# Kernel tuning notes

Hardware: AMD Instinct MI355X
Metric: run time of the kernel (lower is better)

Reference implementation:

```python
import jax, jax.numpy as jnp
import numpy as np

DIM = 768
N_HEADS = 12
HEAD_DIM = DIM // N_HEADS
HIDDEN = int(DIM * 4.0)
B, S = 4, 2048
EPS = 1e-6
SCALE = HEAD_DIM ** -0.5


def layer_norm(x, gamma, beta):
    mu = jnp.mean(x, axis=-1, keepdims=True)
    var = jnp.mean((x - mu) ** 2, axis=-1, keepdims=True)
    return (x - mu) * jax.lax.rsqrt(var + EPS) * gamma + beta


def setup_inputs() -> dict:
    key = jax.random.key(0)
    ks = jax.random.split(key, 8)
    x = jax.random.normal(ks[0], (B, S, DIM), dtype=jnp.float32)
    mask = jax.random.randint(ks[1], (B, 1, S, S), 0, 2, dtype=jnp.int32)
    sd = DIM ** -0.5
    return {
        "x": x,
        "mask": mask,
        "w_qkv": jax.random.normal(ks[2], (DIM, 3 * DIM), dtype=jnp.float32) * sd,
        "b_qkv": jnp.zeros((3 * DIM,), jnp.float32),
        "w_proj": jax.random.normal(ks[3], (DIM, DIM), dtype=jnp.float32) * sd,
        "b_proj": jnp.zeros((DIM,), jnp.float32),
        "g1": jnp.ones((DIM,), jnp.float32),
        "beta1": jnp.zeros((DIM,), jnp.float32),
        "g2": jnp.ones((DIM,), jnp.float32),
        "beta2": jnp.zeros((DIM,), jnp.float32),
        "w1": jax.random.normal(ks[4], (DIM, HIDDEN), dtype=jnp.float32) * sd,
        "b1": jnp.zeros((HIDDEN,), jnp.float32),
        "w2": jax.random.normal(ks[5], (HIDDEN, DIM), dtype=jnp.float32) * (HIDDEN ** -0.5),
        "b2": jnp.zeros((DIM,), jnp.float32),
    }


def reference(x, mask, w_qkv, b_qkv, w_proj, b_proj, g1, beta1, g2, beta2, w1, b1, w2, b2):
    # --- attention branch (pre-LN) ---
    h = layer_norm(x, g1, beta1)
    qkv = h @ w_qkv + b_qkv                              # (B,S,3*DIM)
    qkv = qkv.reshape(B, S, 3, N_HEADS, HEAD_DIM)
    q, k, v = (qkv[:, :, 0], qkv[:, :, 1], qkv[:, :, 2])  # (B,S,H,D)
    # scores: (B,H,S,S) -- materialized like the original
    dp = jnp.einsum("bqhd,bkhd->bhqk", q, k) * SCALE
    dp = jnp.where(mask == 0, jnp.float32(-10000.0), dp)
    attn = jax.nn.softmax(dp, axis=-1)
    wa = jnp.einsum("bhqk,bkhd->bqhd", attn, v).reshape(B, S, DIM)
    x = x + (wa @ w_proj + b_proj)
    # --- MLP branch (pre-LN) ---
    h = layer_norm(x, g2, beta2)
    h = jax.nn.gelu(h @ w1 + b1, approximate=False)
    x = x + (h @ w2 + b2)
    return x
```

## Files before the change

kernel.cpp:

```cpp
#include <hip/hip_runtime.h>
#include <math.h>

typedef __bf16 bf16;
typedef __bf16 bf16x8 __attribute__((ext_vector_type(8)));
typedef float f32x4 __attribute__((ext_vector_type(4)));

#define DIM 768
#define NH 12
#define HD 64
#define HID 3072
#define BB 4
#define SS 2048
#define SCALE_QK 0.125f
#define QPRESCALE 0.18033688011112042f

#define MFMA(a, b, c) __builtin_amdgcn_mfma_f32_16x16x32_bf16(a, b, c, 0, 0, 0)

__device__ __forceinline__ void gld16(const void* g, void* l) {
  __builtin_amdgcn_global_load_lds(
      (const __attribute__((address_space(1))) void*)g,
      (__attribute__((address_space(3))) void*)l, 16, 0, 0);
}

__global__ __launch_bounds__(256) void castT_kernel(
    const float* __restrict__ in, bf16* __restrict__ out, int R, int C) {
  __shared__ float tile[32][33];
  const int c0 = blockIdx.x * 32, r0 = blockIdx.y * 32;
  const int tx = threadIdx.x & 31, ty = threadIdx.x >> 5;
#pragma unroll
  for (int i = 0; i < 32; i += 8)
    tile[ty + i][tx] = in[(size_t)(r0 + ty + i) * C + c0 + tx];
  __syncthreads();
#pragma unroll
  for (int i = 0; i < 32; i += 8)
    out[(size_t)(c0 + ty + i) * R + r0 + tx] = (bf16)tile[tx][ty + i];
}

__global__ __launch_bounds__(256) void maskbits_kernel(
    const int* __restrict__ mask, unsigned* __restrict__ bits) {
  const int i = blockIdx.x * 256 + threadIdx.x;
  unsigned long long m = __ballot(mask[i] != 0);
  const int lane = threadIdx.x & 63;
  if (lane == 0) bits[i >> 5] = (unsigned)m;
  else if (lane == 32) bits[i >> 5] = (unsigned)(m >> 32);
}

__global__ __launch_bounds__(256) void ln_kernel(
    const float* __restrict__ x, const float* __restrict__ g,
    const float* __restrict__ beta, bf16* __restrict__ out) {
  const int row = blockIdx.x, t = threadIdx.x;
  const float* xr = x + (size_t)row * DIM;
  float v0 = xr[t], v1 = xr[t + 256], v2 = xr[t + 512];
  float s = v0 + v1 + v2;
  float s2 = v0 * v0 + v1 * v1 + v2 * v2;
#pragma unroll
  for (int d = 1; d < 64; d <<= 1) {
    s += __shfl_xor(s, d);
    s2 += __shfl_xor(s2, d);
  }
  __shared__ float red[8];
  const int wv = t >> 6, lane = t & 63;
  if (lane == 0) { red[wv] = s; red[wv + 4] = s2; }
  __syncthreads();
  s = red[0] + red[1] + red[2] + red[3];
  s2 = red[4] + red[5] + red[6] + red[7];
  const float mu = s * (1.0f / DIM);
  const float var = s2 * (1.0f / DIM) - mu * mu;
  const float r = rsqrtf(var + 1e-6f);
  bf16* o = out + (size_t)row * DIM;
  o[t] = (bf16)((v0 - mu) * r * g[t] + beta[t]);
  o[t + 256] = (bf16)((v1 - mu) * r * g[t + 256] + beta[t + 256]);
  o[t + 512] = (bf16)((v2 - mu) * r * g[t + 512] + beta[t + 512]);
}

enum { EPI_QKV = 0, EPI_PROJ = 1, EPI_FFN1 = 2, EPI_FFN2 = 3 };

template <int EPI, int K>
__global__ __launch_bounds__(256) void gemm_kernel(
    const bf16* __restrict__ A, const bf16* __restrict__ Bt,
    const float* __restrict__ bias, const float* __restrict__ res,
    void* __restrict__ o0, void* __restrict__ o1, void* __restrict__ o2) {
  __shared__ bf16 As[128 * 64];
  __shared__ bf16 Bs[128 * 64];
  const int tid = threadIdx.x;
  const int wv = tid >> 6, lane = tid & 63;
  const int quad = lane >> 4, l15 = lane & 15;
  const int lrow = lane >> 3, lcol = lane & 7;
  const int m0 = blockIdx.y * 128, n0 = blockIdx.x * 128;
  const int wm = (wv >> 1) * 64, wn = (wv & 1) * 64;

  f32x4 acc[4][4] = {};

  const int swz = (lcol ^ lrow) * 8;
  const bf16* Ag = A + (size_t)(m0 + wv * 32 + lrow) * K + swz;
  const bf16* Bg = Bt + (size_t)(n0 + wv * 32 + lrow) * K + swz;
  bf16* Al = As + (wv * 32) * 64;
  bf16* Bl = Bs + (wv * 32) * 64;

  for (int k0 = 0; k0 < K; k0 += 64) {
#pragma unroll
    for (int i = 0; i < 4; i++) {
      gld16(Ag + (size_t)(i * 8) * K + k0, Al + i * 8 * 64);
      gld16(Bg + (size_t)(i * 8) * K + k0, Bl + i * 8 * 64);
    }
    __syncthreads();
#pragma unroll
    for (int ks = 0; ks < 2; ks++) {
      bf16x8 af[4], bfr[4];
#pragma unroll
      for (int i = 0; i < 4; i++) {
        const int ra = wm + i * 16 + l15;
        af[i] = *(const bf16x8*)&As[ra * 64 + ((ks * 4 + quad) ^ (ra & 7)) * 8];
        const int rb = wn + i * 16 + l15;
        bfr[i] = *(const bf16x8*)&Bs[rb * 64 + ((ks * 4 + quad) ^ (rb & 7)) * 8];
      }
#pragma unroll
      for (int mi = 0; mi < 4; mi++)
#pragma unroll
        for (int ni = 0; ni < 4; ni++)
          acc[mi][ni] = MFMA(af[mi], bfr[ni], acc[mi][ni]);
    }
    __syncthreads();
  }

#pragma unroll
  for (int mi = 0; mi < 4; mi++) {
#pragma unroll
    for (int ni = 0; ni < 4; ni++) {
      const int n = n0 + wn + ni * 16 + l15;
      const float bv = bias[n];
      const int mb = m0 + wm + mi * 16 + quad * 4;
#pragma unroll
      for (int r = 0; r < 4; r++) {
        const int m = mb + r;
        const float val = acc[mi][ni][r] + bv;
        if (EPI == EPI_QKV) {
          const int which = n / 768;
          const int nn = n - which * 768;
          const int hh = nn >> 6, d = nn & 63;
          const int bb = m >> 11, s = m & 2047;
          if (which == 0) {
            ((bf16*)o0)[((size_t)(bb * NH + hh) * SS + s) * HD + d] =
                (bf16)(val * QPRESCALE);
          } else if (which == 1) {
            ((bf16*)o1)[((size_t)(bb * NH + hh) * SS + s) * HD + d] = (bf16)val;
          } else {
            ((bf16*)o2)[((size_t)(bb * NH + hh) * HD + d) * SS + s] = (bf16)val;
          }
        } else if (EPI == EPI_PROJ) {
          ((float*)o0)[(size_t)m * DIM + n] = res[(size_t)m * DIM + n] + val;
        } else if (EPI == EPI_FFN1) {
          const float ge = 0.5f * val * (1.0f + erff(val * 0.70710678118654752f));
          ((bf16*)o0)[(size_t)m * HID + n] = (bf16)ge;
        } else {
          ((float*)o0)[(size_t)m * DIM + n] = res[(size_t)m * DIM + n] + val;
        }
      }
    }
  }
}

__global__ __launch_bounds__(256) void attn_kernel(
    const bf16* __restrict__ q, const bf16* __restrict__ k,
    const bf16* __restrict__ vT, const unsigned* __restrict__ bits,
    bf16* __restrict__ wa) {
  const int b = blockIdx.z, h = blockIdx.y, q0 = blockIdx.x * 128;
  const int tid = threadIdx.x, wv = tid >> 6, lane = tid & 63;
  const int quad = lane >> 4, l15 = lane & 15;
  const int lrow = lane >> 3, lcol = lane & 7;

  __shared__ bf16 Ks[64 * 64];
  __shared__ bf16 Vs[64 * 64];
  __shared__ bf16 Ps[4][32 * 64];

  const bf16* qbh = q + (size_t)(b * NH + h) * SS * HD;
  const bf16* kbh = k + (size_t)(b * NH + h) * SS * HD;
  const bf16* vbh = vT + (size_t)(b * NH + h) * HD * SS;

  bf16x8 aq[2][2];
#pragma unroll
  for (int mi = 0; mi < 2; mi++)
#pragma unroll
    for (int ks = 0; ks < 2; ks++) {
      const int s = q0 + wv * 32 + mi * 16 + l15;
      aq[mi][ks] = *(const bf16x8*)&qbh[(size_t)s * HD + ks * 32 + quad * 8];
    }

  float lsum[2][4];
  f32x4 O[2][4] = {};
#pragma unroll
  for (int mi = 0; mi < 2; mi++)
#pragma unroll
    for (int r = 0; r < 4; r++) lsum[mi][r] = 0.0f;

  bf16* P = Ps[wv];
  const int swz = (lcol ^ lrow) * 8;
  const unsigned* bitrow =
      bits + (size_t)(b * SS + q0 + wv * 32 + quad * 4) * 64;

  for (int s0 = 0; s0 < SS; s0 += 64) {
#pragma unroll
    for (int i = 0; i < 2; i++) {
      const int r = wv * 16 + i * 8 + lrow;
      gld16(&kbh[(size_t)(s0 + r) * HD + swz], &Ks[(wv * 16 + i * 8) * 64]);
      gld16(&vbh[(size_t)r * SS + s0 + swz], &Vs[(wv * 16 + i * 8) * 64]);
    }

    unsigned long long ww[2][4];
#pragma unroll
    for (int mi = 0; mi < 2; mi++)
#pragma unroll
      for (int r = 0; r < 4; r++)
        ww[mi][r] = *(const unsigned long long*)&bitrow[(size_t)(mi * 16 + r) * 64 + (s0 >> 5)];

    __syncthreads();

    bf16x8 bk[4][2], bv[4][2];
#pragma unroll
    for (int ni = 0; ni < 4; ni++)
#pragma unroll
      for (int ks = 0; ks < 2; ks++) {
        const int rr = ni * 16 + l15;
        const int sl = ((ks * 4 + quad) ^ (rr & 7)) * 8;
        bk[ni][ks] = *(const bf16x8*)&Ks[rr * 64 + sl];
        bv[ni][ks] = *(const bf16x8*)&Vs[rr * 64 + sl];
      }

    f32x4 sc[2][4];
#pragma unroll
    for (int mi = 0; mi < 2; mi++)
#pragma unroll
      for (int ni = 0; ni < 4; ni++) {
        f32x4 a = {};
        a = MFMA(aq[mi][0], bk[ni][0], a);
        a = MFMA(aq[mi][1], bk[ni][1], a);
        sc[mi][ni] = a;
      }

#pragma unroll
    for (int mi = 0; mi < 2; mi++)
#pragma unroll
      for (int r = 0; r < 4; r++) {
        const unsigned long long sh = ww[mi][r] >> l15;
        const unsigned lo = (unsigned)sh, hi = (unsigned)(sh >> 32);
        float ls = lsum[mi][r];
#pragma unroll
        for (int ni = 0; ni < 4; ni++) {
          const unsigned bit =
              (ni == 0) ? (lo & 1u) : (ni == 1) ? ((lo >> 16) & 1u)
                        : (ni == 2) ? (hi & 1u) : ((hi >> 16) & 1u);
          float pv = __builtin_amdgcn_exp2f(sc[mi][ni][r]);
          pv = bit ? pv : 0.0f;
          sc[mi][ni][r] = pv;
          ls += pv;
        }
        lsum[mi][r] = ls;
      }

#pragma unroll
    for (int mi = 0; mi < 2; mi++)
#pragma unroll
      for (int ni = 0; ni < 4; ni++)
#pragma unroll
        for (int r = 0; r < 4; r++) {
          const int row = mi * 16 + quad * 4 + r;
          const int col = ni * 16 + l15;
          const int sl = (col >> 3) ^ (row & 7);
          P[row * 64 + sl * 8 + (col & 7)] = (bf16)sc[mi][ni][r];
        }

    bf16x8 ap[2][2];
#pragma unroll
    for (int mi = 0; mi < 2; mi++)
#pragma unroll
      for (int ks = 0; ks < 2; ks++) {
        const int rr = mi * 16 + l15;
        const int sl = ((ks * 4 + quad) ^ (rr & 7)) * 8;
        ap[mi][ks] = *(const bf16x8*)&P[rr * 64 + sl];
      }
#pragma unroll
    for (int mi = 0; mi < 2; mi++)
#pragma unroll
      for (int nd = 0; nd < 4; nd++) {
        O[mi][nd] = MFMA(ap[mi][0], bv[nd][0], O[mi][nd]);
        O[mi][nd] = MFMA(ap[mi][1], bv[nd][1], O[mi][nd]);
      }
    __syncthreads();
  }

  float rln[2][4];
#pragma unroll
  for (int mi = 0; mi < 2; mi++)
#pragma unroll
    for (int r = 0; r < 4; r++) {
      float ls = lsum[mi][r];
      ls += __shfl_xor(ls, 1);
      ls += __shfl_xor(ls, 2);
      ls += __shfl_xor(ls, 4);
      ls += __shfl_xor(ls, 8);
      rln[mi][r] = __builtin_amdgcn_rcpf(ls);
    }

#pragma unroll
  for (int mi = 0; mi < 2; mi++)
#pragma unroll
    for (int nd = 0; nd < 4; nd++)
#pragma unroll
      for (int r = 0; r < 4; r++) {
        const int s = q0 + wv * 32 + mi * 16 + quad * 4 + r;
        const int n = h * HD + nd * 16 + l15;
        wa[(size_t)(b * SS + s) * DIM + n] = (bf16)(O[mi][nd][r] * rln[mi][r]);
      }
}

extern "C" void kernel_launch(void* const* d_in, const int* in_sizes, int n_in,
                              void* d_out, int out_size, void* d_ws,
                              size_t ws_size, hipStream_t stream) {
  const float* x = (const float*)d_in[0];
  const int* mask = (const int*)d_in[1];
  const float* w_qkv = (const float*)d_in[2];
  const float* b_qkv = (const float*)d_in[3];
  const float* w_proj = (const float*)d_in[4];
  const float* b_proj = (const float*)d_in[5];
  const float* g1 = (const float*)d_in[6];
  const float* beta1 = (const float*)d_in[7];
  const float* g2 = (const float*)d_in[8];
  const float* beta2 = (const float*)d_in[9];
  const float* w1 = (const float*)d_in[10];
  const float* b1 = (const float*)d_in[11];
  const float* w2 = (const float*)d_in[12];
  const float* b2 = (const float*)d_in[13];
  float* out = (float*)d_out;

  char* p = (char*)d_ws;
  auto alloc = [&](size_t bytes) {
    char* r = p;
    p += (bytes + 1023) & ~(size_t)1023;
    return r;
  };
  bf16* wqkvT = (bf16*)alloc((size_t)2304 * 768 * 2);
  bf16* wprojT = (bf16*)alloc((size_t)768 * 768 * 2);
  bf16* w1T = (bf16*)alloc((size_t)3072 * 768 * 2);
  bf16* w2T = (bf16*)alloc((size_t)768 * 3072 * 2);
  unsigned* bits = (unsigned*)alloc((size_t)BB * SS * 64 * 4);
  bf16* h = (bf16*)alloc((size_t)8192 * 768 * 2);
  bf16* qb = (bf16*)alloc((size_t)8192 * 768 * 2);
  bf16* kb = (bf16*)alloc((size_t)8192 * 768 * 2);
  bf16* vtb = (bf16*)alloc((size_t)8192 * 768 * 2);
  bf16* wab = (bf16*)alloc((size_t)8192 * 768 * 2);
  float* x2 = (float*)alloc((size_t)8192 * 768 * 4);
  bf16* ffn1 = (bf16*)alloc((size_t)8192 * 3072 * 2);

  castT_kernel<<<dim3(2304 / 32, 768 / 32), 256, 0, stream>>>(w_qkv, wqkvT, 768, 2304);
  castT_kernel<<<dim3(768 / 32, 768 / 32), 256, 0, stream>>>(w_proj, wprojT, 768, 768);
  castT_kernel<<<dim3(3072 / 32, 768 / 32), 256, 0, stream>>>(w1, w1T, 768, 3072);
  castT_kernel<<<dim3(768 / 32, 3072 / 32), 256, 0, stream>>>(w2, w2T, 3072, 768);
  maskbits_kernel<<<(BB * SS * SS) / 256, 256, 0, stream>>>(mask, bits);
  ln_kernel<<<8192, 256, 0, stream>>>(x, g1, beta1, h);
  gemm_kernel<EPI_QKV, 768><<<dim3(2304 / 128, 8192 / 128), 256, 0, stream>>>(
      h, wqkvT, b_qkv, nullptr, qb, kb, vtb);
  attn_kernel<<<dim3(SS / 128, NH, BB), 256, 0, stream>>>(qb, kb, vtb, bits, wab);
  gemm_kernel<EPI_PROJ, 768><<<dim3(768 / 128, 8192 / 128), 256, 0, stream>>>(
      wab, wprojT, b_proj, x, x2, nullptr, nullptr);
  ln_kernel<<<8192, 256, 0, stream>>>(x2, g2, beta2, h);
  gemm_kernel<EPI_FFN1, 768><<<dim3(3072 / 128, 8192 / 128), 256, 0, stream>>>(
      h, w1T, b1, nullptr, ffn1, nullptr, nullptr);
  gemm_kernel<EPI_FFN2, 3072><<<dim3(768 / 128, 8192 / 128), 256, 0, stream>>>(
      ffn1, w2T, b2, x2, out, nullptr, nullptr);
}
```

Baseline: 541.9 us.

## Rewrite attention to keep P in registers via transposed MFMA, merge weight casts

The attention kernel now computes S^T by swapping the MFMA operands, so each lane holds one query row's probabilities. It feeds them straight into 16x16x16 MFMAs against V, which drops the LDS staging of K, V and P and removes both block barriers. K and V fragments are loaded directly from global memory per wave rather than shared through LDS, which raises global/L2 traffic per block. The four weight cast-transpose launches are merged into one kernel, and the V^T store in the QKV epilogue is packed into 8-byte writes.

Result: slower. 671.8 us (+24.0%).

```diff
diff --git a/kernel.cpp b/kernel.cpp
--- a/kernel.cpp
+++ b/kernel.cpp
@@ -1,8 +1,10 @@
 #include <hip/hip_runtime.h>
+#include <hip/hip_bf16.h>
 #include <math.h>
 
 typedef __bf16 bf16;
 typedef __bf16 bf16x8 __attribute__((ext_vector_type(8)));
+typedef short bf16x4s __attribute__((ext_vector_type(4)));
 typedef float f32x4 __attribute__((ext_vector_type(4)));
 
 #define DIM 768
@@ -15,6 +17,8 @@
 #define QPRESCALE 0.18033688011112042f
 
 #define MFMA(a, b, c) __builtin_amdgcn_mfma_f32_16x16x32_bf16(a, b, c, 0, 0, 0)
+#define MFMA16(a, b, c) \
+  __builtin_amdgcn_mfma_f32_16x16x16bf16_1k(a, b, c, 0, 0, 0)
 
 __device__ __forceinline__ void gld16(const void* g, void* l) {
   __builtin_amdgcn_global_load_lds(
@@ -22,10 +26,32 @@
       (__attribute__((address_space(3))) void*)l, 16, 0, 0);
 }
 
-__global__ __launch_bounds__(256) void castT_kernel(
-    const float* __restrict__ in, bf16* __restrict__ out, int R, int C) {
+__device__ __forceinline__ unsigned pk2(float a, float b) {
+  union {
+    bf16 h[2];
+    unsigned u;
+  } t;
+  t.h[0] = (bf16)a;
+  t.h[1] = (bf16)b;
+  return t.u;
+}
+
+__global__ __launch_bounds__(256) void castT_all_kernel(
+    const float* __restrict__ s0, bf16* __restrict__ d0,
+    const float* __restrict__ s1, bf16* __restrict__ d1,
+    const float* __restrict__ s2, bf16* __restrict__ d2,
+    const float* __restrict__ s3, bf16* __restrict__ d3) {
   __shared__ float tile[32][33];
-  const int c0 = blockIdx.x * 32, r0 = blockIdx.y * 32;
+  int id = blockIdx.x;
+  const float* in;
+  bf16* out;
+  int R, C, loc;
+  if (id < 1728) { in = s0; out = d0; R = 768; C = 2304; loc = id; }
+  else if (id < 2304) { in = s1; out = d1; R = 768; C = 768; loc = id - 1728; }
+  else if (id < 4608) { in = s2; out = d2; R = 768; C = 3072; loc = id - 2304; }
+  else { in = s3; out = d3; R = 3072; C = 768; loc = id - 4608; }
+  const int cb = C >> 5;
+  const int c0 = (loc % cb) * 32, r0 = (loc / cb) * 32;
   const int tx = threadIdx.x & 31, ty = threadIdx.x >> 5;
 #pragma unroll
   for (int i = 0; i < 32; i += 8)
@@ -130,31 +156,47 @@
       const int n = n0 + wn + ni * 16 + l15;
       const float bv = bias[n];
       const int mb = m0 + wm + mi * 16 + quad * 4;
-#pragma unroll
-      for (int r = 0; r < 4; r++) {
-        const int m = mb + r;
-        const float val = acc[mi][ni][r] + bv;
-        if (EPI == EPI_QKV) {
-          const int which = n / 768;
-          const int nn = n - which * 768;
-          const int hh = nn >> 6, d = nn & 63;
-          const int bb = m >> 11, s = m & 2047;
-          if (which == 0) {
-            ((bf16*)o0)[((size_t)(bb * NH + hh) * SS + s) * HD + d] =
-                (bf16)(val * QPRESCALE);
-          } else if (which == 1) {
-            ((bf16*)o1)[((size_t)(bb * NH + hh) * SS + s) * HD + d] = (bf16)val;
-          } else {
-            ((bf16*)o2)[((size_t)(bb * NH + hh) * HD + d) * SS + s] = (bf16)val;
-          }
-        } else if (EPI == EPI_PROJ) {
-          ((float*)o0)[(size_t)m * DIM + n] = res[(size_t)m * DIM + n] + val;
-        } else if (EPI == EPI_FFN1) {
-          const float ge = 0.5f * val * (1.0f + erff(val * 0.70710678118654752f));
-          ((bf16*)o0)[(size_t)m * HID + n] = (bf16)ge;
+      float val[4];
+#pragma unroll
+      for (int r = 0; r < 4; r++) val[r] = acc[mi][ni][r] + bv;
+      if (EPI == EPI_QKV) {
+        const int which = n / 768;
+        const int nn = n - which * 768;
+        const int hh = nn >> 6, d = nn & 63;
+        const int bb = mb >> 11, s = mb & 2047;
+        if (which == 0) {
+#pragma unroll
+          for (int r = 0; r < 4; r++)
+            ((bf16*)o0)[((size_t)(bb * NH + hh) * SS + s + r) * HD + d] =
+                (bf16)(val[r] * QPRESCALE);
+        } else if (which == 1) {
+#pragma unroll
+          for (int r = 0; r < 4; r++)
+            ((bf16*)o1)[((size_t)(bb * NH + hh) * SS + s + r) * HD + d] =
+                (bf16)val[r];
         } else {
-          ((float*)o0)[(size_t)m * DIM + n] = res[(size_t)m * DIM + n] + val;
+          uint2 pv;
+          pv.x = pk2(val[0], val[1]);
+          pv.y = pk2(val[2], val[3]);
+          *(uint2*)&((bf16*)o2)[((size_t)(bb * NH + hh) * HD + d) * SS + s] = pv;
         }
+      } else if (EPI == EPI_PROJ) {
+#pragma unroll
+        for (int r = 0; r < 4; r++)
+          ((float*)o0)[(size_t)(mb + r) * DIM + n] =
+              res[(size_t)(mb + r) * DIM + n] + val[r];
+      } else if (EPI == EPI_FFN1) {
+#pragma unroll
+        for (int r = 0; r < 4; r++) {
+          const float ge =
+              0.5f * val[r] * (1.0f + erff(val[r] * 0.70710678118654752f));
+          ((bf16*)o0)[(size_t)(mb + r) * HID + n] = (bf16)ge;
+        }
+      } else {
+#pragma unroll
+        for (int r = 0; r < 4; r++)
+          ((float*)o0)[(size_t)(mb + r) * DIM + n] =
+              res[(size_t)(mb + r) * DIM + n] + val[r];
       }
     }
   }
@@ -167,11 +209,6 @@
   const int b = blockIdx.z, h = blockIdx.y, q0 = blockIdx.x * 128;
   const int tid = threadIdx.x, wv = tid >> 6, lane = tid & 63;
   const int quad = lane >> 4, l15 = lane & 15;
-  const int lrow = lane >> 3, lcol = lane & 7;
-
-  __shared__ bf16 Ks[64 * 64];
-  __shared__ bf16 Vs[64 * 64];
-  __shared__ bf16 Ps[4][32 * 64];
 
   const bf16* qbh = q + (size_t)(b * NH + h) * SS * HD;
   const bf16* kbh = k + (size_t)(b * NH + h) * SS * HD;
@@ -186,131 +223,89 @@
       aq[mi][ks] = *(const bf16x8*)&qbh[(size_t)s * HD + ks * 32 + quad * 8];
     }
 
-  float lsum[2][4];
+  const unsigned long long* mptr[2];
+#pragma unroll
+  for (int mi = 0; mi < 2; mi++)
+    mptr[mi] = (const unsigned long long*)bits +
+               (size_t)(b * SS + q0 + wv * 32 + mi * 16 + l15) * 32;
+
+  float lsum[2] = {0.0f, 0.0f};
   f32x4 O[2][4] = {};
-#pragma unroll
-  for (int mi = 0; mi < 2; mi++)
-#pragma unroll
-    for (int r = 0; r < 4; r++) lsum[mi][r] = 0.0f;
-
-  bf16* P = Ps[wv];
-  const int swz = (lcol ^ lrow) * 8;
-  const unsigned* bitrow =
-      bits + (size_t)(b * SS + q0 + wv * 32 + quad * 4) * 64;
 
   for (int s0 = 0; s0 < SS; s0 += 64) {
-#pragma unroll
-    for (int i = 0; i < 2; i++) {
-      const int r = wv * 16 + i * 8 + lrow;
-      gld16(&kbh[(size_t)(s0 + r) * HD + swz], &Ks[(wv * 16 + i * 8) * 64]);
-      gld16(&vbh[(size_t)r * SS + s0 + swz], &Vs[(wv * 16 + i * 8) * 64]);
-    }
-
-    unsigned long long ww[2][4];
-#pragma unroll
-    for (int mi = 0; mi < 2; mi++)
-#pragma unroll
-      for (int r = 0; r < 4; r++)
-        ww[mi][r] = *(const unsigned long long*)&bitrow[(size_t)(mi * 16 + r) * 64 + (s0 >> 5)];
-
-    __syncthreads();
-
-    bf16x8 bk[4][2], bv[4][2];
+    bf16x8 kf[4][2];
 #pragma unroll
     for (int ni = 0; ni < 4; ni++)
 #pragma unroll
-      for (int ks = 0; ks < 2; ks++) {
-        const int rr = ni * 16 + l15;
-        const int sl = ((ks * 4 + quad) ^ (rr & 7)) * 8;
-        bk[ni][ks] = *(const bf16x8*)&Ks[rr * 64 + sl];
-        bv[ni][ks] = *(const bf16x8*)&Vs[rr * 64 + sl];
-      }
-
-    f32x4 sc[2][4];
-#pragma unroll
-    for (int mi = 0; mi < 2; mi++)
+      for (int ks = 0; ks < 2; ks++)
+        kf[ni][ks] = *(const bf16x8*)&kbh[(size_t)(s0 + ni * 16 + l15) * HD +
+                                          ks * 32 + quad * 8];
+    bf16x4s vf[4][4];
+#pragma unroll
+    for (int nd = 0; nd < 4; nd++)
+#pragma unroll
+      for (int ni = 0; ni < 4; ni++)
+        vf[nd][ni] = *(const bf16x4s*)&vbh[(size_t)(nd * 16 + l15) * SS + s0 +
+                                           ni * 16 + quad * 4];
+    const unsigned long long ww[2] = {mptr[0][s0 >> 6] >> (quad * 4),
+                                      mptr[1][s0 >> 6] >> (quad * 4)};
+
+    unsigned pf[2][4][2];
+#pragma unroll
+    for (int mi = 0; mi < 2; mi++) {
+      const unsigned long long sh = ww[mi];
+      float ls = lsum[mi];
 #pragma unroll
       for (int ni = 0; ni < 4; ni++) {
         f32x4 a = {};
-        a = MFMA(aq[mi][0], bk[ni][0], a);
-        a = MFMA(aq[mi][1], bk[ni][1], a);
-        sc[mi][ni] = a;
+        a = MFMA(kf[ni][0], aq[mi][0], a);
+        a = MFMA(kf[ni][1], aq[mi][1], a);
+        float pv[4];
+#pragma unroll
+        for (int r = 0; r < 4; r++) {
+          const unsigned bit = (unsigned)(sh >> (ni * 16 + r)) & 1u;
+          const float p = bit ? __builtin_amdgcn_exp2f(a[r]) : 0.0f;
+          pv[r] = p;
+          ls += p;
+        }
+        pf[mi][ni][0] = pk2(pv[0], pv[1]);
+        pf[mi][ni][1] = pk2(pv[2], pv[3]);
       }
+      lsum[mi] = ls;
+    }
 
 #pragma unroll
     for (int mi = 0; mi < 2; mi++)
 #pragma unroll
-      for (int r = 0; r < 4; r++) {
-        const unsigned long long sh = ww[mi][r] >> l15;
-        const unsigned lo = (unsigned)sh, hi = (unsigned)(sh >> 32);
-        float ls = lsum[mi][r];
+      for (int nd = 0; nd < 4; nd++)
 #pragma unroll
         for (int ni = 0; ni < 4; ni++) {
-          const unsigned bit =
-              (ni == 0) ? (lo & 1u) : (ni == 1) ? ((lo >> 16) & 1u)
-                        : (ni == 2) ? (hi & 1u) : ((hi >> 16) & 1u);
-          float pv = __builtin_amdgcn_exp2f(sc[mi][ni][r]);
-          pv = bit ? pv : 0.0f;
-          sc[mi][ni][r] = pv;
-          ls += pv;
+          union {
+            unsigned u[2];
+            bf16x4s v;
+          } pp;
+          pp.u[0] = pf[mi][ni][0];
+          pp.u[1] = pf[mi][ni][1];
+          O[mi][nd] = MFMA16(vf[nd][ni], pp.v, O[mi][nd]);
         }
-        lsum[mi][r] = ls;
-      }
-
-#pragma unroll
-    for (int mi = 0; mi < 2; mi++)
-#pragma unroll
-      for (int ni = 0; ni < 4; ni++)
-#pragma unroll
-        for (int r = 0; r < 4; r++) {
-          const int row = mi * 16 + quad * 4 + r;
-          const int col = ni * 16 + l15;
-          const int sl = (col >> 3) ^ (row & 7);
-          P[row * 64 + sl * 8 + (col & 7)] = (bf16)sc[mi][ni][r];
-        }
-
-    bf16x8 ap[2][2];
-#pragma unroll
-    for (int mi = 0; mi < 2; mi++)
-#pragma unroll
-      for (int ks = 0; ks < 2; ks++) {
-        const int rr = mi * 16 + l15;
-        const int sl = ((ks * 4 + quad) ^ (rr & 7)) * 8;
-        ap[mi][ks] = *(const bf16x8*)&P[rr * 64 + sl];
-      }
-#pragma unroll
-    for (int mi = 0; mi < 2; mi++)
-#pragma unroll
-      for (int nd = 0; nd < 4; nd++) {
-        O[mi][nd] = MFMA(ap[mi][0], bv[nd][0], O[mi][nd]);
-        O[mi][nd] = MFMA(ap[mi][1], bv[nd][1], O[mi][nd]);
-      }
-    __syncthreads();
-  }
-
-  float rln[2][4];
-#pragma unroll
-  for (int mi = 0; mi < 2; mi++)
-#pragma unroll
-    for (int r = 0; r < 4; r++) {
-      float ls = lsum[mi][r];
-      ls += __shfl_xor(ls, 1);
-      ls += __shfl_xor(ls, 2);
-      ls += __shfl_xor(ls, 4);
-      ls += __shfl_xor(ls, 8);
-      rln[mi][r] = __builtin_amdgcn_rcpf(ls);
-    }
-
-#pragma unroll
-  for (int mi = 0; mi < 2; mi++)
-#pragma unroll
-    for (int nd = 0; nd < 4; nd++)
-#pragma unroll
-      for (int r = 0; r < 4; r++) {
-        const int s = q0 + wv * 32 + mi * 16 + quad * 4 + r;
-        const int n = h * HD + nd * 16 + l15;
-        wa[(size_t)(b * SS + s) * DIM + n] = (bf16)(O[mi][nd][r] * rln[mi][r]);
-      }
+  }
+
+#pragma unroll
+  for (int mi = 0; mi < 2; mi++) {
+    float ls = lsum[mi];
+    ls += __shfl_xor(ls, 16);
+    ls += __shfl_xor(ls, 32);
+    const float rln = __builtin_amdgcn_rcpf(ls);
+    const int s = q0 + wv * 32 + mi * 16 + l15;
+    bf16* dst = wa + (size_t)(b * SS + s) * DIM + h * HD + quad * 4;
+#pragma unroll
+    for (int nd = 0; nd < 4; nd++) {
+      uint2 pv;
+      pv.x = pk2(O[mi][nd][0] * rln, O[mi][nd][1] * rln);
+      pv.y = pk2(O[mi][nd][2] * rln, O[mi][nd][3] * rln);
+      *(uint2*)&dst[nd * 16] = pv;
+    }
+  }
 }
 
 extern "C" void kernel_launch(void* const* d_in, const int* in_sizes, int n_in,
@@ -351,10 +346,8 @@
   float* x2 = (float*)alloc((size_t)8192 * 768 * 4);
   bf16* ffn1 = (bf16*)alloc((size_t)8192 * 3072 * 2);
 
-  castT_kernel<<<dim3(2304 / 32, 768 / 32), 256, 0, stream>>>(w_qkv, wqkvT, 768, 2304);
-  castT_kernel<<<dim3(768 / 32, 768 / 32), 256, 0, stream>>>(w_proj, wprojT, 768, 768);
-  castT_kernel<<<dim3(3072 / 32, 768 / 32), 256, 0, stream>>>(w1, w1T, 768, 3072);
-  castT_kernel<<<dim3(768 / 32, 3072 / 32), 256, 0, stream>>>(w2, w2T, 3072, 768);
+  castT_all_kernel<<<6912, 256, 0, stream>>>(w_qkv, wqkvT, w_proj, wprojT, w1,
+                                             w1T, w2, w2T);
   maskbits_kernel<<<(BB * SS * SS) / 256, 256, 0, stream>>>(mask, bits);
   ln_kernel<<<8192, 256, 0, stream>>>(x, g1, beta1, h);
   gemm_kernel<EPI_QKV, 768><<<dim3(2304 / 128, 8192 / 128), 256, 0, stream>>>(
```
